# Kernel optimization log

Hardware: AMD Instinct MI355X
Metric: run time of the kernel (lower is better)

The kernel has to match this reference:

```python
import jax, jax.numpy as jnp
import numpy as np

B = 1024      # jets per batch
P = 150       # TOTAL_PARTICLES per jet
N = B * P     # total nodes
DEG = 16      # avg degree
E = N * DEG
H = 256       # GNN_HIDDEN_DIM
K = 6         # GNN_K
NC = 10       # NUM_CLUSTERS
IN = 3


def setup_inputs() -> dict:
    key = jax.random.key(0)
    ks = jax.random.split(key, 16)
    x = jax.random.normal(ks[0], (N, IN), jnp.float32)
    # kNN-like within-jet edges: each node sends to DEG random nodes of its own jet
    src = jnp.repeat(jnp.arange(N, dtype=jnp.int32), DEG)
    tgt = (src // P) * P + jax.random.randint(ks[1], (E,), 0, P, dtype=jnp.int32)
    edge_index = jnp.stack([src, tgt])  # [2, E]
    batch = jnp.arange(N, dtype=jnp.int32) // P  # sorted graph ids, exactly P per graph
    inp = dict(x=x, edge_index=edge_index, batch=batch)
    dims = [(IN, H), (H, H), (H, H), (H, H)]
    for i, (di, do) in enumerate(dims):
        s = 1.0 / np.sqrt(di)
        inp[f"W{i+1}"] = jax.random.uniform(ks[2 + i], (K, di, do), jnp.float32, -s, s)
        inp[f"b{i+1}"] = jnp.zeros((do,), jnp.float32)
    for i in range(3):
        inp[f"g{i+1}"] = jnp.ones((H,), jnp.float32)
        inp[f"be{i+1}"] = jnp.zeros((H,), jnp.float32)
    inp["centers"] = jax.random.normal(ks[10], (NC, 2), jnp.float32) * 0.2
    inp["log_temp"] = jnp.float32(2.0)
    return inp


def _lap_weights(src, tgt, n):
    # PyG ChebConv norm with lambda_max=2, sym normalization, self-loops removed:
    # scaled Laplacian L_hat = -D^{-1/2} A D^{-1/2} (zero diagonal)
    w = (src != tgt).astype(jnp.float32)          # remove self-loops
    deg = jax.ops.segment_sum(w, src, num_segments=n)
    dis = jnp.where(deg > 0, 1.0 / jnp.sqrt(deg), 0.0)
    return -(dis[src] * w * dis[tgt])             # [E]


def _cheb(x, W, b, src, tgt, lw, n):
    # Chebyshev recurrence: T0=x, T1=Lx, Tk=2L T_{k-1} - T_{k-2}
    prop = lambda h: jax.ops.segment_sum(lw[:, None] * h[src], tgt, num_segments=n)
    Tx0 = x
    out = Tx0 @ W[0]
    Tx1 = prop(Tx0)
    out = out + Tx1 @ W[1]
    for k in range(2, W.shape[0]):
        Tx2 = 2.0 * prop(Tx1) - Tx0
        out = out + Tx2 @ W[k]
        Tx0, Tx1 = Tx1, Tx2
    return out + b


def _bn(h, g, b):
    # BatchNorm1d, training-mode batch statistics (biased var), eps=1e-5
    m = h.mean(0)
    v = h.var(0)
    return (h - m) * jax.lax.rsqrt(v + 1e-5) * g + b


def reference(x, edge_index, batch, W1, b1, W2, b2, W3, b3, W4, b4,
              g1, be1, g2, be2, g3, be3, centers, log_temp):
    n = x.shape[0]
    src, tgt = edge_index[0], edge_index[1]
    lw = _lap_weights(src, tgt, n)
    lrelu = lambda h: jax.nn.leaky_relu(h, 0.01)
    h = lrelu(_bn(_cheb(x, W1, b1, src, tgt, lw, n), g1, be1))
    h = lrelu(_bn(_cheb(h, W2, b2, src, tgt, lw, n), g2, be2))
    h = lrelu(_bn(_cheb(h, W3, b3, src, tgt, lw, n), g3, be3))
    h = _cheb(h, W4, b4, src, tgt, lw, n)
    h = h / jnp.maximum(jnp.linalg.norm(h, axis=1, keepdims=True), 1e-12)  # F.normalize
    # to_dense_batch: batch is sorted with exactly P nodes per graph -> pure reshape,
    # node_mask is all True
    dense_h = h.reshape(B, P, -1)          # [B, P, H]
    dense_c = x[:, :2].reshape(B, P, 2)    # (eta, phi)
    dist = ((dense_c[:, :, None, :] - centers) ** 2).sum(-1)   # [B, P, NC]
    T = jnp.exp(jnp.clip(log_temp, -2.0, 3.0))
    assignment = jax.nn.softmax(-T * dist, axis=-1)            # mask is all-true
    pooled = jnp.einsum('bnk,bnd->bkd', assignment, dense_h)   # [B, NC, H]
    pooled = pooled / (assignment.sum(1)[:, :, None] + 1e-8)
    return pooled.reshape(B, -1)  # [B, NC*H]
```

## Files before the change

kernel.cpp:

```cpp
#include <hip/hip_runtime.h>
#include <cstdio>

#define NODES 153600
#define PJ 150
#define NJETS 1024
#define DEG 16
#define NEDGE (NODES*DEG)
#define HD 256
#define NCL 10

#define LSTR 168
#define TSTR 76

typedef unsigned short u16;
typedef _Float16 f16;
typedef f16 f16x8 __attribute__((ext_vector_type(8)));
typedef u16 u16x8 __attribute__((ext_vector_type(8)));
typedef u16 u16x4 __attribute__((ext_vector_type(4)));
typedef float f32x4 __attribute__((ext_vector_type(4)));

__device__ inline float h2f(u16 u) { union { u16 s; f16 h; } v; v.s = u; return (float)v.h; }
__device__ inline u16 f2h(float f) { union { u16 s; f16 h; } v; v.h = (f16)f; return v.s; }

template<typename T> __device__ inline float ldv(const T* p);
template<> __device__ inline float ldv<float>(const float* p) { return *p; }
template<> __device__ inline float ldv<u16>(const u16* p) { return h2f(*p); }
template<typename T> __device__ inline void stv(T* p, float v);
template<> __device__ inline void stv<float>(float* p, float v) { *p = v; }
template<> __device__ inline void stv<u16>(u16* p, float v) { *p = f2h(v); }

__global__ void k_diag(float* out, float code) {
  if (blockIdx.x == 0 && threadIdx.x == 0) out[0] = code;
}


__global__ __launch_bounds__(256) void k_dis(const int* __restrict__ tgt, float* __restrict__ dis) {
  int n = blockIdx.x*256 + threadIdx.x;
  if (n >= NODES) return;
  int cnt = 0;
#pragma unroll
  for (int j = 0; j < DEG; ++j) cnt += (tgt[n*DEG + j] != n) ? 1 : 0;
  dis[n] = (cnt > 0) ? rsqrtf((float)cnt) : 0.f;
}

__global__ __launch_bounds__(256) void k_counts(const int* __restrict__ tgt, int* __restrict__ counts) {
  int e = blockIdx.x*256 + threadIdx.x;
  if (e >= NEDGE) return;
  atomicAdd(&counts[tgt[e]], 1);
}

__global__ __launch_bounds__(256) void k_scan(const int* __restrict__ counts, int* __restrict__ rowptr, int* __restrict__ cursor) {
  int j = blockIdx.x*256 + threadIdx.x;
  if (j >= NJETS) return;
  int run = j*PJ*DEG;
  for (int l = 0; l < PJ; ++l) {
    int idx = j*PJ + l;
    int cnt = counts[idx];
    rowptr[idx] = run;
    cursor[idx] = run;
    run += cnt;
  }
  if (j == 0) rowptr[NODES] = NEDGE;
}

__global__ __launch_bounds__(256) void k_fill(const int* __restrict__ src_, const int* __restrict__ tgt_,
                                              const float* __restrict__ dis, int* __restrict__ cursor,
                                              unsigned char* __restrict__ ccol, float* __restrict__ cw) {
  int e = blockIdx.x*256 + threadIdx.x;
  if (e >= NEDGE) return;
  int s = src_[e], t = tgt_[e];
  int pos = atomicAdd(&cursor[t], 1);
  ccol[pos] = (unsigned char)(s % PJ);
  cw[pos] = (s != t) ? -(dis[s]*dis[t]) : 0.f;
}

__global__ __launch_bounds__(256) void k_prepL(const int* __restrict__ rowptr,
                                               const unsigned char* __restrict__ ccol,
                                               const float* __restrict__ cw,
                                               u16* __restrict__ Lg) {
  int j = blockIdx.x, tid = threadIdx.x;
  u16* L = Lg + (size_t)j*160*160;
  if (tid < 160) {
    u16x8 z = {0,0,0,0,0,0,0,0};
    for (int seg = 0; seg < 20; ++seg) *(u16x8*)&L[tid*160 + seg*8] = z;
    if (tid < PJ) {
      int es = rowptr[j*PJ + tid], ee = rowptr[j*PJ + tid + 1];
      u16* row = L + tid*160;
      for (int e = es; e < ee; ++e) {
        int c = (int)ccol[e];
        row[c] = f2h(h2f(row[c]) + 2.f*cw[e]);
      }
    }
  }
}

__global__ __launch_bounds__(512) void k_cheb3(const float* __restrict__ x,
                                               const int* __restrict__ rowptr,
                                               const unsigned char* __restrict__ ccol,
                                               const float* __restrict__ cw,
                                               float* __restrict__ tall) {
  __shared__ float Ta[450], Tb[450];
  __shared__ float cw_s[PJ*DEG];
  __shared__ u16  col_s[PJ*DEG];
  __shared__ int  rp_s[PJ+1];
  int j = blockIdx.x, tid = threadIdx.x;
  int jb = j*PJ, e0 = jb*DEG;
  for (int i = tid; i < PJ*DEG; i += 512) { cw_s[i] = cw[e0+i]; col_s[i] = (u16)ccol[e0+i]; }
  for (int i = tid; i < PJ+1; i += 512) rp_s[i] = rowptr[jb+i] - e0;
  if (tid < 450) Ta[tid] = x[(size_t)jb*3 + tid];
  __syncthreads();
  int r = tid/3, c = tid - r*3;
  float* cur = Ta; float* oth = Tb;
  if (tid < 450) tall[(size_t)(jb+r)*18 + c] = cur[tid];
  for (int t = 1; t < 6; ++t) {
    if (tid < 450) {
      int es = rp_s[r], ee = rp_s[r+1];
      float acc = 0.f;
      for (int e = es; e < ee; ++e) acc += cw_s[e]*cur[(int)col_s[e]*3 + c];
      float v = (t == 1) ? acc : 2.f*acc - oth[tid];
      oth[tid] = v;
      tall[(size_t)(jb+r)*18 + t*3 + c] = v;
    }
    __syncthreads();
    float* tmp = cur; cur = oth; oth = tmp;
  }
}

template<typename OT>
__global__ __launch_bounds__(256) void k_gemm1(const float* __restrict__ tall, const float* __restrict__ W1,
                                               OT* __restrict__ outc) {
  __shared__ float wl[18*256];
  __shared__ float tl[64*18];
  int c = threadIdx.x;
  for (int i = c; i < 18*256; i += 256) wl[i] = W1[i];
  int n0 = blockIdx.x*64;
  __syncthreads();
  for (int i = c; i < 64*18; i += 256) tl[i] = tall[(size_t)n0*18 + i];
  __syncthreads();
  for (int n = 0; n < 64; ++n) {
    float acc = 0.f;
#pragma unroll
    for (int i = 0; i < 18; ++i) acc += tl[n*18 + i] * wl[i*256 + c];
    stv(&outc[(size_t)(n0+n)*HD + c], acc);
  }
}

__global__ __launch_bounds__(256) void k_prepW(const float* __restrict__ W, u16* __restrict__ WT) {
  int i = blockIdx.x*256 + threadIdx.x;
  if (i >= 256*1536) return;
  int cout = i / 1536, k = i - cout*1536;
  int term = k >> 8, cin = k & 255;
  WT[i] = f2h(W[(size_t)term*65536 + cin*256 + cout]);
}

template<typename OT>
__global__ __launch_bounds__(1024, 4) void k_cheb(const u16* __restrict__ X,
                                                  const u16* __restrict__ WTu,
                                                  const u16* __restrict__ Lg,
                                                  const float* __restrict__ bias,
                                                  float* __restrict__ stats,
                                                  OT* __restrict__ OUTp) {
  __shared__ u16 Ls[160*LSTR];
  __shared__ u16 Tn[2][160*TSTR];
  __shared__ u16 Tt[2][64*LSTR];
  int j = blockIdx.x, tid = threadIdx.x;
  int jb = j*PJ;
  int lane = tid & 63, wid = tid >> 6;
  int wm = wid >> 3, wn = wid & 7;
  int lr = lane & 15, lg = lane >> 4;
  int ph = wn >> 2, cs = wn & 3;
  int cown = cs*16 + lr;
  const f16* WT = (const f16*)WTu;

  {
    const u16* src = Lg + (size_t)j*25600;
    for (int i = tid; i < 3200; i += 1024) {
      int row = i/20, seg = i - row*20;
      *(u16x8*)&Ls[row*LSTR + seg*8] = *(const u16x8*)&src[row*160 + seg*8];
    }
  }
  f32x4 acc[5][2];
#pragma unroll
  for (int a = 0; a < 5; ++a)
#pragma unroll
    for (int b = 0; b < 2; ++b) acc[a][b] = (f32x4)0.f;

  for (int qp = 0; qp < 2; ++qp) {
    __syncthreads();
    for (int i = tid; i < 2560; i += 1024) {
      int h = (i >= 1280) ? 1 : 0;
      int rem = i - h*1280;
      int row = rem >> 3, seg = rem & 7;
      u16x8 v = {0,0,0,0,0,0,0,0};
      if (row < PJ) v = *(const u16x8*)&X[(size_t)(jb+row)*HD + (qp*2+h)*64 + seg*8];
      *(u16x8*)&Tn[h][row*TSTR + seg*8] = v;
    }
    __syncthreads();
    for (int i = tid; i < 2560; i += 1024) {
      int h = (i >= 1280) ? 1 : 0;
      int rem = i - h*1280;
      int c = rem & 63, m = rem >> 6;
      u16x8 v;
#pragma unroll
      for (int u = 0; u < 8; ++u) v[u] = Tn[h][(m*8+u)*TSTR + c];
      *(u16x8*)&Tt[h][c*LSTR + m*8] = v;
    }
    u16x4 tcur[5], tprev[5];
#pragma unroll
    for (int mf = 0; mf < 5; ++mf) {
      int r0 = wm*80 + mf*16 + lg*4;
#pragma unroll
      for (int e = 0; e < 4; ++e) tcur[mf][e] = Tn[ph][(r0+e)*TSTR + cown];
      tprev[mf] = tcur[mf];
    }
    __syncthreads();
#pragma unroll 1
    for (int t = 0; t < 6; ++t) {
#pragma unroll
      for (int h = 0; h < 2; ++h) {
        int kbase = t*256 + (qp*2+h)*64;
#pragma unroll
        for (int ks = 0; ks < 64; ks += 32) {
          f16x8 a[5], bv[2];
#pragma unroll
          for (int nf = 0; nf < 2; ++nf)
            bv[nf] = *(const f16x8*)&WT[(size_t)(wn*32 + nf*16 + lr)*1536 + kbase + ks + lg*8];
#pragma unroll
          for (int mf = 0; mf < 5; ++mf)
            a[mf] = *(const f16x8*)&Tn[h][(wm*80 + mf*16 + lr)*TSTR + ks + lg*8];
#pragma unroll
          for (int nf = 0; nf < 2; ++nf)
#pragma unroll
            for (int mf = 0; mf < 5; ++mf)
              acc[mf][nf] = __builtin_amdgcn_mfma_f32_16x16x32_f16(a[mf], bv[nf], acc[mf][nf], 0, 0, 0);
        }
      }
      if (t < 5) {
        f32x4 pacc[5];
#pragma unroll
        for (int mf = 0; mf < 5; ++mf) pacc[mf] = (f32x4)0.f;
#pragma unroll
        for (int ks = 0; ks < 5; ++ks) {
          f16x8 b = *(const f16x8*)&Tt[ph][cown*LSTR + ks*32 + lg*8];
#pragma unroll
          for (int mf = 0; mf < 5; ++mf) {
            f16x8 a = *(const f16x8*)&Ls[(wm*80 + mf*16 + lr)*LSTR + ks*32 + lg*8];
            pacc[mf] = __builtin_amdgcn_mfma_f32_16x16x32_f16(a, b, pacc[mf], 0, 0, 0);
          }
        }
        __syncthreads();
#pragma unroll
        for (int mf = 0; mf < 5; ++mf) {
          int r0 = wm*80 + mf*16 + lg*4;
          u16x4 o;
#pragma unroll
          for (int e = 0; e < 4; ++e) {
            float v = (t == 0) ? 0.5f*pacc[mf][e]
                               : pacc[mf][e] - h2f(tprev[mf][e]);
            o[e] = f2h(v);
            Tn[ph][(r0+e)*TSTR + cown] = o[e];
          }
          *(u16x4*)&Tt[ph][cown*LSTR + r0] = o;
          tprev[mf] = tcur[mf];
          tcur[mf] = o;
        }
        __syncthreads();
      }
    }
  }
#pragma unroll
  for (int nf = 0; nf < 2; ++nf) {
    int col = wn*32 + nf*16 + lr;
    float bc = bias[col];
    float s = 0.f, s2 = 0.f;
#pragma unroll
    for (int mf = 0; mf < 5; ++mf) {
      int row = wm*80 + mf*16 + lg*4;
#pragma unroll
      for (int e = 0; e < 4; ++e) {
        int r = row + e;
        if (r < PJ) {
          float v = acc[mf][nf][e];
          stv(&OUTp[(size_t)(jb+r)*HD + col], v);
          float vb = v + bc;
          s += vb; s2 += vb*vb;
        }
      }
    }
    s  += __shfl_xor(s, 16, 64);  s  += __shfl_xor(s, 32, 64);
    s2 += __shfl_xor(s2, 16, 64); s2 += __shfl_xor(s2, 32, 64);
    if (lg == 0) {
      atomicAdd(&stats[col], s);
      atomicAdd(&stats[HD + col], s2);
    }
  }
}


template<typename OT>
__global__ __launch_bounds__(256) void k_bnstats(const OT* __restrict__ Cc, const float* __restrict__ bias,
                                                 float* __restrict__ stats) {
  int c = threadIdx.x;
  float bc = bias[c];
  float s = 0.f, s2 = 0.f;
  int rows_per = (NODES + gridDim.x - 1) / gridDim.x;
  int r0 = blockIdx.x * rows_per;
  int r1 = min(NODES, r0 + rows_per);
  for (int r = r0; r < r1; ++r) {
    float v = ldv(&Cc[(size_t)r*HD + c]) + bc;
    s += v; s2 += v*v;
  }
  atomicAdd(&stats[c], s);
  atomicAdd(&stats[HD + c], s2);
}

template<typename OT>
__global__ __launch_bounds__(256) void k_bnapply(const OT* __restrict__ Cc, const float* __restrict__ bias,
                                                 const float* __restrict__ stats, const float* __restrict__ g,
                                                 const float* __restrict__ be, u16* __restrict__ hout) {
  const float invN = 1.f/(float)NODES;
  int total = NODES*HD;
  for (int i = blockIdx.x*256 + threadIdx.x; i < total; i += gridDim.x*256) {
    int c = i & (HD-1);
    float m = stats[c]*invN;
    float v = stats[HD+c]*invN - m*m;
    float wq = rsqrtf(v + 1e-5f);
    float val = (ldv(&Cc[i]) + bias[c] - m)*wq*g[c] + be[c];
    hout[i] = f2h((val > 0.f) ? val : 0.01f*val);
  }
}


template<typename OT>
__global__ __launch_bounds__(256) void k_rownorm(const OT* __restrict__ Cc, const float* __restrict__ bias,
                                                 u16* __restrict__ hout) {
  int wave = threadIdx.x >> 6, lane = threadIdx.x & 63;
  int n = blockIdx.x*4 + wave;
  float v0 = ldv(&Cc[(size_t)n*HD + lane*4 + 0]) + bias[lane*4 + 0];
  float v1 = ldv(&Cc[(size_t)n*HD + lane*4 + 1]) + bias[lane*4 + 1];
  float v2 = ldv(&Cc[(size_t)n*HD + lane*4 + 2]) + bias[lane*4 + 2];
  float v3 = ldv(&Cc[(size_t)n*HD + lane*4 + 3]) + bias[lane*4 + 3];
  float ss = v0*v0 + v1*v1 + v2*v2 + v3*v3;
  for (int off = 32; off > 0; off >>= 1) ss += __shfl_down(ss, off, 64);
  ss = __shfl(ss, 0, 64);
  float inv = 1.f / fmaxf(sqrtf(ss), 1e-12f);
  hout[(size_t)n*HD + lane*4 + 0] = f2h(v0*inv);
  hout[(size_t)n*HD + lane*4 + 1] = f2h(v1*inv);
  hout[(size_t)n*HD + lane*4 + 2] = f2h(v2*inv);
  hout[(size_t)n*HD + lane*4 + 3] = f2h(v3*inv);
}


__global__ __launch_bounds__(256) void k_pool(const u16* __restrict__ h, const float* __restrict__ x,
                                              const float* __restrict__ centers, const float* __restrict__ log_temp,
                                              float* __restrict__ out) {
  __shared__ float a_s[PJ][NCL];
  __shared__ float colsum[NCL];
  int j = blockIdx.x;
  int tid = threadIdx.x;
  float T = expf(fminf(fmaxf(log_temp[0], -2.f), 3.f));
  if (tid < PJ) {
    int g = j*PJ + tid;
    float eta = x[(size_t)g*3], phi = x[(size_t)g*3 + 1];
    float d[NCL];
    float dmin = 1e30f;
#pragma unroll
    for (int k = 0; k < NCL; ++k) {
      float dx = eta - centers[2*k], dy = phi - centers[2*k+1];
      d[k] = dx*dx + dy*dy;
      dmin = fminf(dmin, d[k]);
    }
    float s = 0.f, ek[NCL];
#pragma unroll
    for (int k = 0; k < NCL; ++k) { ek[k] = expf(-T*(d[k]-dmin)); s += ek[k]; }
    float invs = 1.f/s;
#pragma unroll
    for (int k = 0; k < NCL; ++k) a_s[tid][k] = ek[k]*invs;
  }
  __syncthreads();
  if (tid < NCL) {
    float s = 0.f;
    for (int n = 0; n < PJ; ++n) s += a_s[n][tid];
    colsum[tid] = s;
  }
  __syncthreads();
  int c = tid;
  float acc[NCL] = {};
  for (int n = 0; n < PJ; ++n) {
    float hv = h2f(h[(size_t)(j*PJ + n)*HD + c]);
#pragma unroll
    for (int k = 0; k < NCL; ++k) acc[k] += a_s[n][k]*hv;
  }
#pragma unroll
  for (int k = 0; k < NCL; ++k)
    out[(size_t)j*(NCL*HD) + k*HD + c] = acc[k] / (colsum[k] + 1e-8f);
}


template<typename OT>
static void run_plan(const float* x, const int* srcA, const int* tgtA,
                     const float* W1, const float* b1, const float* W2, const float* b2,
                     const float* W3, const float* b3, const float* W4, const float* b4,
                     const float* g1, const float* be1, const float* g2, const float* be2,
                     const float* g3, const float* be3, const float* centers, const float* log_temp,
                     float* out, char* wp0, hipStream_t stream) {
  char* wp = wp0;
  auto alloc = [&](size_t b) -> void* {
    void* p = (void*)wp;
    wp += (b + 255) & ~(size_t)255;
    return p;
  };
  u16*   X    = (u16*)alloc((size_t)NODES*HD*2);
  u16*   Y    = (u16*)alloc((size_t)NODES*HD*2);
  OT*    OUT  = (OT*)alloc((size_t)NODES*HD*sizeof(OT));
  float* dis  = (float*)alloc((size_t)NODES*4);
  int*   counts = (int*)alloc((size_t)NODES*4);
  int*   cursor = (int*)alloc((size_t)NODES*4);
  int*   rowptr = (int*)alloc((size_t)(NODES+1)*4);
  unsigned char* ccol = (unsigned char*)alloc((size_t)NEDGE);
  float* cw     = (float*)alloc((size_t)NEDGE*4);
  float* stats  = (float*)alloc((size_t)2*HD*4);
  float* Tall = (float*)Y;
  u16*   Lg   = Y;
  u16*   Wcat = Y + (size_t)NJETS*160*160;

  hipMemsetAsync(counts, 0, (size_t)NODES*4, stream);
  k_dis<<<(NODES+255)/256, 256, 0, stream>>>(tgtA, dis);
  k_counts<<<(NEDGE+255)/256, 256, 0, stream>>>(tgtA, counts);
  k_scan<<<(NJETS+255)/256, 256, 0, stream>>>(counts, rowptr, cursor);
  k_fill<<<(NEDGE+255)/256, 256, 0, stream>>>(srcA, tgtA, dis, cursor, ccol, cw);

  k_cheb3<<<NJETS, 512, 0, stream>>>(x, rowptr, ccol, cw, Tall);
  k_gemm1<OT><<<NODES/64, 256, 0, stream>>>(Tall, W1, OUT);
  hipMemsetAsync(stats, 0, (size_t)2*HD*4, stream);
  k_bnstats<OT><<<1024, 256, 0, stream>>>(OUT, b1, stats);
  k_bnapply<OT><<<4096, 256, 0, stream>>>(OUT, b1, stats, g1, be1, X);

  k_prepL<<<NJETS, 256, 0, stream>>>(rowptr, ccol, cw, Lg);

  const float* Ws[3]  = {W2, W3, W4};
  const float* bs[3]  = {b2, b3, b4};
  const float* gs[2]  = {g2, g3};
  const float* bes[2] = {be2, be3};
  for (int L = 0; L < 3; ++L) {
    k_prepW<<<1536, 256, 0, stream>>>(Ws[L], Wcat);
    hipMemsetAsync(stats, 0, (size_t)2*HD*4, stream);
    k_cheb<OT><<<NJETS, 1024, 0, stream>>>(X, Wcat, Lg, bs[L], stats, OUT);
    if (L < 2) {
      k_bnapply<OT><<<4096, 256, 0, stream>>>(OUT, bs[L], stats, gs[L], bes[L], X);
    } else {
      k_rownorm<OT><<<NODES/4, 256, 0, stream>>>(OUT, bs[L], X);
    }
  }

  k_pool<<<NJETS, 256, 0, stream>>>(X, x, centers, log_temp, out);
}

extern "C" void kernel_launch(void* const* d_in, const int* in_sizes, int n_in,
                              void* d_out, int out_size, void* d_ws, size_t ws_size,
                              hipStream_t stream) {
  (void)in_sizes; (void)n_in; (void)out_size;
  const float* x   = (const float*)d_in[0];
  const int*   ei  = (const int*)d_in[1];
  const int*   srcA = ei;
  const int*   tgtA = ei + NEDGE;
  const float* W1  = (const float*)d_in[3];
  const float* b1  = (const float*)d_in[4];
  const float* W2  = (const float*)d_in[5];
  const float* b2  = (const float*)d_in[6];
  const float* W3  = (const float*)d_in[7];
  const float* b3  = (const float*)d_in[8];
  const float* W4  = (const float*)d_in[9];
  const float* b4  = (const float*)d_in[10];
  const float* g1  = (const float*)d_in[11];
  const float* be1 = (const float*)d_in[12];
  const float* g2  = (const float*)d_in[13];
  const float* be2 = (const float*)d_in[14];
  const float* g3  = (const float*)d_in[15];
  const float* be3 = (const float*)d_in[16];
  const float* centers  = (const float*)d_in[17];
  const float* log_temp = (const float*)d_in[18];
  float* out = (float*)d_out;

  auto rb = [](size_t b) { return (b + 255) & ~(size_t)255; };
  auto plan_bytes = [&](size_t out_esz) {
    return 2*rb((size_t)NODES*HD*2) + rb((size_t)NODES*HD*out_esz)
         + 3*rb((size_t)NODES*4) + rb((size_t)(NODES+1)*4)
         + rb((size_t)NEDGE) + rb((size_t)NEDGE*4) + rb((size_t)2*HD*4);
  };
  size_t needA = plan_bytes(4);
  size_t needB = plan_bytes(2);
  fprintf(stderr, "[kernel_launch] ws_size=%zu needA=%zu needB=%zu\n", ws_size, needA, needB);

  if (d_ws == nullptr || ws_size < needB) {
    float code = 1.0e6f + (float)(ws_size >> 20);
    k_diag<<<1, 1, 0, stream>>>(out, code);
    return;
  }

  if (ws_size >= needA)
    run_plan<float>(x, srcA, tgtA, W1, b1, W2, b2, W3, b3, W4, b4,
                    g1, be1, g2, be2, g3, be3, centers, log_temp,
                    out, (char*)d_ws, stream);
  else
    run_plan<u16>(x, srcA, tgtA, W1, b1, W2, b2, W3, b3, W4, b4,
                  g1, be1, g2, be2, g3, be3, centers, log_temp,
                  out, (char*)d_ws, stream);
}
```

Measured before the change: 1.544 ms.

## Fuse BatchNorm apply and row-norm into Chebyshev kernels, drop separate passes

The BatchNorm scale/shift and leaky ReLU are applied while the next Chebyshev layer loads its input tile, and the BN statistics for layer 1 are accumulated inside the first GEMM. The final layer accumulates per-row squared norms with atomics so that pooling can apply the bias and normalization itself. This removes the standalone bnstats, bnapply and rownorm kernels and their full-tensor HBM round trips, and intermediates are now always stored in fp16. TSTR padding also changes from 76 to 72, which may alter LDS bank conflicts, and the extra atomics add contention.

```diff
diff --git a/kernel.cpp b/kernel.cpp
--- a/kernel.cpp
+++ b/kernel.cpp
@@ -10,7 +10,7 @@
 #define NCL 10
 
 #define LSTR 168
-#define TSTR 76
+#define TSTR 72
 
 typedef unsigned short u16;
 typedef _Float16 f16;
@@ -21,13 +21,6 @@
 
 __device__ inline float h2f(u16 u) { union { u16 s; f16 h; } v; v.s = u; return (float)v.h; }
 __device__ inline u16 f2h(float f) { union { u16 s; f16 h; } v; v.h = (f16)f; return v.s; }
-
-template<typename T> __device__ inline float ldv(const T* p);
-template<> __device__ inline float ldv<float>(const float* p) { return *p; }
-template<> __device__ inline float ldv<u16>(const u16* p) { return h2f(*p); }
-template<typename T> __device__ inline void stv(T* p, float v);
-template<> __device__ inline void stv<float>(float* p, float v) { *p = v; }
-template<> __device__ inline void stv<u16>(u16* p, float v) { *p = f2h(v); }
 
 __global__ void k_diag(float* out, float code) {
   if (blockIdx.x == 0 && threadIdx.x == 0) out[0] = code;
@@ -126,9 +119,9 @@
   }
 }
 
-template<typename OT>
 __global__ __launch_bounds__(256) void k_gemm1(const float* __restrict__ tall, const float* __restrict__ W1,
-                                               OT* __restrict__ outc) {
+                                               const float* __restrict__ b1, float* __restrict__ stats,
+                                               u16* __restrict__ outc) {
   __shared__ float wl[18*256];
   __shared__ float tl[64*18];
   int c = threadIdx.x;
@@ -137,12 +130,18 @@
   __syncthreads();
   for (int i = c; i < 64*18; i += 256) tl[i] = tall[(size_t)n0*18 + i];
   __syncthreads();
+  float bc = b1[c];
+  float s = 0.f, s2 = 0.f;
   for (int n = 0; n < 64; ++n) {
     float acc = 0.f;
 #pragma unroll
     for (int i = 0; i < 18; ++i) acc += tl[n*18 + i] * wl[i*256 + c];
-    stv(&outc[(size_t)(n0+n)*HD + c], acc);
-  }
+    outc[(size_t)(n0+n)*HD + c] = f2h(acc);
+    float vb = acc + bc;
+    s += vb; s2 += vb*vb;
+  }
+  atomicAdd(&stats[c], s);
+  atomicAdd(&stats[HD + c], s2);
 }
 
 __global__ __launch_bounds__(256) void k_prepW(const float* __restrict__ W, u16* __restrict__ WT) {
@@ -153,16 +152,22 @@
   WT[i] = f2h(W[(size_t)term*65536 + cin*256 + cout]);
 }
 
-template<typename OT>
-__global__ __launch_bounds__(1024, 4) void k_cheb(const u16* __restrict__ X,
+template<int OMODE>
+__global__ __launch_bounds__(1024, 4) void k_cheb(const u16* __restrict__ IN,
                                                   const u16* __restrict__ WTu,
                                                   const u16* __restrict__ Lg,
-                                                  const float* __restrict__ bias,
-                                                  float* __restrict__ stats,
-                                                  OT* __restrict__ OUTp) {
+                                                  const float* __restrict__ statsPrev,
+                                                  const float* __restrict__ gP,
+                                                  const float* __restrict__ beP,
+                                                  const float* __restrict__ bP,
+                                                  const float* __restrict__ bCur,
+                                                  float* __restrict__ statsCur,
+                                                  float* __restrict__ rn,
+                                                  u16* __restrict__ OUTp) {
   __shared__ u16 Ls[160*LSTR];
   __shared__ u16 Tn[2][160*TSTR];
   __shared__ u16 Tt[2][64*LSTR];
+  __shared__ float bnA[HD], bnB[HD];
   int j = blockIdx.x, tid = threadIdx.x;
   int jb = j*PJ;
   int lane = tid & 63, wid = tid >> 6;
@@ -172,6 +177,14 @@
   int cown = cs*16 + lr;
   const f16* WT = (const f16*)WTu;
 
+  if (tid < HD) {
+    const float invN = 1.f/(float)NODES;
+    float m = statsPrev[tid]*invN;
+    float var = statsPrev[HD+tid]*invN - m*m;
+    float A = rsqrtf(var + 1e-5f) * gP[tid];
+    bnA[tid] = A;
+    bnB[tid] = (bP[tid] - m)*A + beP[tid];
+  }
   {
     const u16* src = Lg + (size_t)j*25600;
     for (int i = tid; i < 3200; i += 1024) {
@@ -191,9 +204,17 @@
       int h = (i >= 1280) ? 1 : 0;
       int rem = i - h*1280;
       int row = rem >> 3, seg = rem & 7;
-      u16x8 v = {0,0,0,0,0,0,0,0};
-      if (row < PJ) v = *(const u16x8*)&X[(size_t)(jb+row)*HD + (qp*2+h)*64 + seg*8];
-      *(u16x8*)&Tn[h][row*TSTR + seg*8] = v;
+      u16x8 o = {0,0,0,0,0,0,0,0};
+      if (row < PJ) {
+        int c0 = (qp*2+h)*64 + seg*8;
+        u16x8 v = *(const u16x8*)&IN[(size_t)(jb+row)*HD + c0];
+#pragma unroll
+        for (int u = 0; u < 8; ++u) {
+          float f = h2f(v[u])*bnA[c0+u] + bnB[c0+u];
+          o[u] = f2h((f > 0.f) ? f : 0.01f*f);
+        }
+      }
+      *(u16x8*)&Tn[h][row*TSTR + seg*8] = o;
     }
     __syncthreads();
     for (int i = tid; i < 2560; i += 1024) {
@@ -268,99 +289,78 @@
       }
     }
   }
-#pragma unroll
-  for (int nf = 0; nf < 2; ++nf) {
-    int col = wn*32 + nf*16 + lr;
-    float bc = bias[col];
-    float s = 0.f, s2 = 0.f;
+  if (OMODE == 0) {
+#pragma unroll
+    for (int nf = 0; nf < 2; ++nf) {
+      int col = wn*32 + nf*16 + lr;
+      float bc = bCur[col];
+      float s = 0.f, s2 = 0.f;
+#pragma unroll
+      for (int mf = 0; mf < 5; ++mf) {
+        int row = wm*80 + mf*16 + lg*4;
+#pragma unroll
+        for (int e = 0; e < 4; ++e) {
+          int r = row + e;
+          if (r < PJ) {
+            float v = acc[mf][nf][e];
+            OUTp[(size_t)(jb+r)*HD + col] = f2h(v);
+            float vb = v + bc;
+            s += vb; s2 += vb*vb;
+          }
+        }
+      }
+      s  += __shfl_xor(s, 16, 64);  s  += __shfl_xor(s, 32, 64);
+      s2 += __shfl_xor(s2, 16, 64); s2 += __shfl_xor(s2, 32, 64);
+      if (lg == 0) {
+        atomicAdd(&statsCur[col], s);
+        atomicAdd(&statsCur[HD + col], s2);
+      }
+    }
+  } else {
+    float bc[2];
+#pragma unroll
+    for (int nf = 0; nf < 2; ++nf) bc[nf] = bCur[wn*32 + nf*16 + lr];
 #pragma unroll
     for (int mf = 0; mf < 5; ++mf) {
       int row = wm*80 + mf*16 + lg*4;
 #pragma unroll
       for (int e = 0; e < 4; ++e) {
         int r = row + e;
+        float srow = 0.f;
         if (r < PJ) {
-          float v = acc[mf][nf][e];
-          stv(&OUTp[(size_t)(jb+r)*HD + col], v);
-          float vb = v + bc;
-          s += vb; s2 += vb*vb;
-        }
-      }
-    }
-    s  += __shfl_xor(s, 16, 64);  s  += __shfl_xor(s, 32, 64);
-    s2 += __shfl_xor(s2, 16, 64); s2 += __shfl_xor(s2, 32, 64);
-    if (lg == 0) {
-      atomicAdd(&stats[col], s);
-      atomicAdd(&stats[HD + col], s2);
-    }
-  }
-}
-
-
-template<typename OT>
-__global__ __launch_bounds__(256) void k_bnstats(const OT* __restrict__ Cc, const float* __restrict__ bias,
-                                                 float* __restrict__ stats) {
-  int c = threadIdx.x;
-  float bc = bias[c];
-  float s = 0.f, s2 = 0.f;
-  int rows_per = (NODES + gridDim.x - 1) / gridDim.x;
-  int r0 = blockIdx.x * rows_per;
-  int r1 = min(NODES, r0 + rows_per);
-  for (int r = r0; r < r1; ++r) {
-    float v = ldv(&Cc[(size_t)r*HD + c]) + bc;
-    s += v; s2 += v*v;
-  }
-  atomicAdd(&stats[c], s);
-  atomicAdd(&stats[HD + c], s2);
-}
-
-template<typename OT>
-__global__ __launch_bounds__(256) void k_bnapply(const OT* __restrict__ Cc, const float* __restrict__ bias,
-                                                 const float* __restrict__ stats, const float* __restrict__ g,
-                                                 const float* __restrict__ be, u16* __restrict__ hout) {
-  const float invN = 1.f/(float)NODES;
-  int total = NODES*HD;
-  for (int i = blockIdx.x*256 + threadIdx.x; i < total; i += gridDim.x*256) {
-    int c = i & (HD-1);
-    float m = stats[c]*invN;
-    float v = stats[HD+c]*invN - m*m;
-    float wq = rsqrtf(v + 1e-5f);
-    float val = (ldv(&Cc[i]) + bias[c] - m)*wq*g[c] + be[c];
-    hout[i] = f2h((val > 0.f) ? val : 0.01f*val);
-  }
-}
-
-
-template<typename OT>
-__global__ __launch_bounds__(256) void k_rownorm(const OT* __restrict__ Cc, const float* __restrict__ bias,
-                                                 u16* __restrict__ hout) {
-  int wave = threadIdx.x >> 6, lane = threadIdx.x & 63;
-  int n = blockIdx.x*4 + wave;
-  float v0 = ldv(&Cc[(size_t)n*HD + lane*4 + 0]) + bias[lane*4 + 0];
-  float v1 = ldv(&Cc[(size_t)n*HD + lane*4 + 1]) + bias[lane*4 + 1];
-  float v2 = ldv(&Cc[(size_t)n*HD + lane*4 + 2]) + bias[lane*4 + 2];
-  float v3 = ldv(&Cc[(size_t)n*HD + lane*4 + 3]) + bias[lane*4 + 3];
-  float ss = v0*v0 + v1*v1 + v2*v2 + v3*v3;
-  for (int off = 32; off > 0; off >>= 1) ss += __shfl_down(ss, off, 64);
-  ss = __shfl(ss, 0, 64);
-  float inv = 1.f / fmaxf(sqrtf(ss), 1e-12f);
-  hout[(size_t)n*HD + lane*4 + 0] = f2h(v0*inv);
-  hout[(size_t)n*HD + lane*4 + 1] = f2h(v1*inv);
-  hout[(size_t)n*HD + lane*4 + 2] = f2h(v2*inv);
-  hout[(size_t)n*HD + lane*4 + 3] = f2h(v3*inv);
-}
-
-
-__global__ __launch_bounds__(256) void k_pool(const u16* __restrict__ h, const float* __restrict__ x,
+#pragma unroll
+          for (int nf = 0; nf < 2; ++nf) {
+            int col = wn*32 + nf*16 + lr;
+            float v = acc[mf][nf][e];
+            OUTp[(size_t)(jb+r)*HD + col] = f2h(v);
+            float vb = v + bc[nf];
+            srow += vb*vb;
+          }
+        }
+        srow += __shfl_xor(srow, 1, 64);
+        srow += __shfl_xor(srow, 2, 64);
+        srow += __shfl_xor(srow, 4, 64);
+        srow += __shfl_xor(srow, 8, 64);
+        if (lr == 0 && r < PJ) atomicAdd(&rn[jb + r], srow);
+      }
+    }
+  }
+}
+
+
+__global__ __launch_bounds__(256) void k_pool(const u16* __restrict__ h, const float* __restrict__ rn,
+                                              const float* __restrict__ bias, const float* __restrict__ x,
                                               const float* __restrict__ centers, const float* __restrict__ log_temp,
                                               float* __restrict__ out) {
   __shared__ float a_s[PJ][NCL];
   __shared__ float colsum[NCL];
+  __shared__ float inv_s[PJ];
   int j = blockIdx.x;
   int tid = threadIdx.x;
   float T = expf(fminf(fmaxf(log_temp[0], -2.f), 3.f));
   if (tid < PJ) {
     int g = j*PJ + tid;
+    inv_s[tid] = 1.f / fmaxf(sqrtf(rn[g]), 1e-12f);
     float eta = x[(size_t)g*3], phi = x[(size_t)g*3 + 1];
     float d[NCL];
     float dmin = 1e30f;
@@ -385,9 +385,10 @@
   }
   __syncthreads();
   int c = tid;
+  float bc = bias[c];
   float acc[NCL] = {};
   for (int n = 0; n < PJ; ++n) {
-    float hv = h2f(h[(size_t)(j*PJ + n)*HD + c]);
+    float hv = (h2f(h[(size_t)(j*PJ + n)*HD + c]) + bc) * inv_s[n];
 #pragma unroll
     for (int k = 0; k < NCL; ++k) acc[k] += a_s[n][k]*hv;
   }
@@ -396,65 +397,6 @@
     out[(size_t)j*(NCL*HD) + k*HD + c] = acc[k] / (colsum[k] + 1e-8f);
 }
 
-
-template<typename OT>
-static void run_plan(const float* x, const int* srcA, const int* tgtA,
-                     const float* W1, const float* b1, const float* W2, const float* b2,
-                     const float* W3, const float* b3, const float* W4, const float* b4,
-                     const float* g1, const float* be1, const float* g2, const float* be2,
-                     const float* g3, const float* be3, const float* centers, const float* log_temp,
-                     float* out, char* wp0, hipStream_t stream) {
-  char* wp = wp0;
-  auto alloc = [&](size_t b) -> void* {
-    void* p = (void*)wp;
-    wp += (b + 255) & ~(size_t)255;
-    return p;
-  };
-  u16*   X    = (u16*)alloc((size_t)NODES*HD*2);
-  u16*   Y    = (u16*)alloc((size_t)NODES*HD*2);
-  OT*    OUT  = (OT*)alloc((size_t)NODES*HD*sizeof(OT));
-  float* dis  = (float*)alloc((size_t)NODES*4);
-  int*   counts = (int*)alloc((size_t)NODES*4);
-  int*   cursor = (int*)alloc((size_t)NODES*4);
-  int*   rowptr = (int*)alloc((size_t)(NODES+1)*4);
-  unsigned char* ccol = (unsigned char*)alloc((size_t)NEDGE);
-  float* cw     = (float*)alloc((size_t)NEDGE*4);
-  float* stats  = (float*)alloc((size_t)2*HD*4);
-  float* Tall = (float*)Y;
-  u16*   Lg   = Y;
-  u16*   Wcat = Y + (size_t)NJETS*160*160;
-
-  hipMemsetAsync(counts, 0, (size_t)NODES*4, stream);
-  k_dis<<<(NODES+255)/256, 256, 0, stream>>>(tgtA, dis);
-  k_counts<<<(NEDGE+255)/256, 256, 0, stream>>>(tgtA, counts);
-  k_scan<<<(NJETS+255)/256, 256, 0, stream>>>(counts, rowptr, cursor);
-  k_fill<<<(NEDGE+255)/256, 256, 0, stream>>>(srcA, tgtA, dis, cursor, ccol, cw);
-
-  k_cheb3<<<NJETS, 512, 0, stream>>>(x, rowptr, ccol, cw, Tall);
-  k_gemm1<OT><<<NODES/64, 256, 0, stream>>>(Tall, W1, OUT);
-  hipMemsetAsync(stats, 0, (size_t)2*HD*4, stream);
-  k_bnstats<OT><<<1024, 256, 0, stream>>>(OUT, b1, stats);
-  k_bnapply<OT><<<4096, 256, 0, stream>>>(OUT, b1, stats, g1, be1, X);
-
-  k_prepL<<<NJETS, 256, 0, stream>>>(rowptr, ccol, cw, Lg);
-
-  const float* Ws[3]  = {W2, W3, W4};
-  const float* bs[3]  = {b2, b3, b4};
-  const float* gs[2]  = {g2, g3};
-  const float* bes[2] = {be2, be3};
-  for (int L = 0; L < 3; ++L) {
-    k_prepW<<<1536, 256, 0, stream>>>(Ws[L], Wcat);
-    hipMemsetAsync(stats, 0, (size_t)2*HD*4, stream);
-    k_cheb<OT><<<NJETS, 1024, 0, stream>>>(X, Wcat, Lg, bs[L], stats, OUT);
-    if (L < 2) {
-      k_bnapply<OT><<<4096, 256, 0, stream>>>(OUT, bs[L], stats, gs[L], bes[L], X);
-    } else {
-      k_rownorm<OT><<<NODES/4, 256, 0, stream>>>(OUT, bs[L], X);
-    }
-  }
-
-  k_pool<<<NJETS, 256, 0, stream>>>(X, x, centers, log_temp, out);
-}
 
 extern "C" void kernel_launch(void* const* d_in, const int* in_sizes, int n_in,
                               void* d_out, int out_size, void* d_ws, size_t ws_size,
@@ -483,27 +425,63 @@
   float* out = (float*)d_out;
 
   auto rb = [](size_t b) { return (b + 255) & ~(size_t)255; };
-  auto plan_bytes = [&](size_t out_esz) {
-    return 2*rb((size_t)NODES*HD*2) + rb((size_t)NODES*HD*out_esz)
-         + 3*rb((size_t)NODES*4) + rb((size_t)(NODES+1)*4)
-         + rb((size_t)NEDGE) + rb((size_t)NEDGE*4) + rb((size_t)2*HD*4);
-  };
-  size_t needA = plan_bytes(4);
-  size_t needB = plan_bytes(2);
-  fprintf(stderr, "[kernel_launch] ws_size=%zu needA=%zu needB=%zu\n", ws_size, needA, needB);
-
-  if (d_ws == nullptr || ws_size < needB) {
+  size_t need = 3*rb((size_t)NODES*HD*2)
+              + 3*rb((size_t)NODES*4)
+              + rb((size_t)(NODES+1)*4)
+              + rb((size_t)NEDGE)
+              + rb((size_t)NEDGE*4)
+              + rb((size_t)3*2*HD*4)
+              + rb((size_t)NODES*4);
+  fprintf(stderr, "[kernel_launch] ws_size=%zu need=%zu\n", ws_size, need);
+  if (d_ws == nullptr || ws_size < need) {
     float code = 1.0e6f + (float)(ws_size >> 20);
     k_diag<<<1, 1, 0, stream>>>(out, code);
     return;
   }
 
-  if (ws_size >= needA)
-    run_plan<float>(x, srcA, tgtA, W1, b1, W2, b2, W3, b3, W4, b4,
-                    g1, be1, g2, be2, g3, be3, centers, log_temp,
-                    out, (char*)d_ws, stream);
-  else
-    run_plan<u16>(x, srcA, tgtA, W1, b1, W2, b2, W3, b3, W4, b4,
-                  g1, be1, g2, be2, g3, be3, centers, log_temp,
-                  out, (char*)d_ws, stream);
-}
+  char* wp = (char*)d_ws;
+  auto alloc = [&](size_t b) -> void* {
+    void* p = (void*)wp;
+    wp += (b + 255) & ~(size_t)255;
+    return p;
+  };
+  u16*   OUTA = (u16*)alloc((size_t)NODES*HD*2);
+  u16*   OUTB = (u16*)alloc((size_t)NODES*HD*2);
+  u16*   Y    = (u16*)alloc((size_t)NODES*HD*2);
+  float* dis  = (float*)alloc((size_t)NODES*4);
+  int*   counts = (int*)alloc((size_t)NODES*4);
+  int*   cursor = (int*)alloc((size_t)NODES*4);
+  int*   rowptr = (int*)alloc((size_t)(NODES+1)*4);
+  unsigned char* ccol = (unsigned char*)alloc((size_t)NEDGE);
+  float* cw     = (float*)alloc((size_t)NEDGE*4);
+  float* stats  = (float*)alloc((size_t)3*2*HD*4);
+  float* rn     = (float*)alloc((size_t)NODES*4);
+  float* Tall = (float*)Y;
+  u16*   Lg   = Y;
+  u16*   Wcat = Y + (size_t)NJETS*160*160;
+  float* s0 = stats, *s1 = stats + 512, *s2 = stats + 1024;
+
+  hipMemsetAsync(counts, 0, (size_t)NODES*4, stream);
+  k_dis<<<(NODES+255)/256, 256, 0, stream>>>(tgtA, dis);
+  k_counts<<<(NEDGE+255)/256, 256, 0, stream>>>(tgtA, counts);
+  k_scan<<<(NJETS+255)/256, 256, 0, stream>>>(counts, rowptr, cursor);
+  k_fill<<<(NEDGE+255)/256, 256, 0, stream>>>(srcA, tgtA, dis, cursor, ccol, cw);
+
+  k_cheb3<<<NJETS, 512, 0, stream>>>(x, rowptr, ccol, cw, Tall);
+  hipMemsetAsync(s0, 0, (size_t)2*HD*4, stream);
+  k_gemm1<<<NODES/64, 256, 0, stream>>>(Tall, W1, b1, s0, OUTA);
+
+  k_prepL<<<NJETS, 256, 0, stream>>>(rowptr, ccol, cw, Lg);
+
+  k_prepW<<<1536, 256, 0, stream>>>(W2, Wcat);
+  hipMemsetAsync(s1, 0, (size_t)2*HD*4, stream);
+  k_cheb<0><<<NJETS, 1024, 0, stream>>>(OUTA, Wcat, Lg, s0, g1, be1, b1, b2, s1, rn, OUTB);
+  k_prepW<<<1536, 256, 0, stream>>>(W3, Wcat);
+  hipMemsetAsync(s2, 0, (size_t)2*HD*4, stream);
+  k_cheb<0><<<NJETS, 1024, 0, stream>>>(OUTB, Wcat, Lg, s1, g2, be2, b2, b3, s2, rn, OUTA);
+  k_prepW<<<1536, 256, 0, stream>>>(W4, Wcat);
+  hipMemsetAsync(rn, 0, (size_t)NODES*4, stream);
+  k_cheb<1><<<NJETS, 1024, 0, stream>>>(OUTA, Wcat, Lg, s2, g3, be3, b3, b4, s2, rn, OUTB);
+
+  k_pool<<<NJETS, 256, 0, stream>>>(OUTB, rn, b4, x, centers, log_temp, out);
+}
```

Measured after the change: 1.388 ms. 1.11x faster.
